# Kernel tuning notes

Hardware: AMD Instinct MI355X
Metric: run time of the kernel (lower is better)

The kernel has to match this reference:

```python
import jax, jax.numpy as jnp
import numpy as np

NLIG = 16384
NPROT = 131072
N = NLIG + NPROT
E = 2097152
B = 256
H = 64


def setup_inputs() -> dict:
    key = jax.random.key(0)
    ks = jax.random.split(key, 40)
    i = iter(range(40))

    def nrm(shape, scale=0.1):
        return (jax.random.normal(ks[next(i)], shape, jnp.float32) * scale)

    inp = {
        'lig_pos': nrm((NLIG, 3), 1.0),
        'lig_feat': nrm((NLIG, 15), 1.0),
        'prot_pos': nrm((NPROT, 3), 1.0),
        'prot_feat': nrm((NPROT, 8), 1.0),
        't': jax.random.uniform(ks[next(i)], (B,), jnp.float32) * 1000.0,
        'lig_batch': jnp.sort(jax.random.randint(ks[next(i)], (NLIG,), 0, B)),
        'prot_batch': jnp.sort(jax.random.randint(ks[next(i)], (NPROT,), 0, B)),
        'edge_index': jax.random.randint(ks[next(i)], (2, E), 0, N),
        'W_lig': nrm((15, H)), 'b_lig': nrm((H,)),
        'W_prot': nrm((8, H)), 'b_prot': nrm((H,)),
        'Wt1': nrm((H, H)), 'bt1': nrm((H,)),
        'Wt2': nrm((H, H)), 'bt2': nrm((H,)),
        'Wrel1': nrm((H, H)), 'brel1': nrm((H,)), 'Wroot1': nrm((H, H)),
        'Wrel2': nrm((H, H)), 'brel2': nrm((H,)), 'Wroot2': nrm((H, H)),
        'Wrel3': nrm((H, H)), 'brel3': nrm((H,)), 'Wroot3': nrm((H, H)),
        'Wro1': nrm((H, H)), 'bro1': nrm((H,)),
        'Wro2': nrm((H, 1)), 'bro2': nrm((1,)),
    }
    return inp


def _time_embedding(t, dim):
    half = dim // 2
    freqs = jnp.exp(jnp.arange(half, dtype=jnp.float32) * (-np.log(10000.0) / (half - 1)))
    e = t[:, None] * freqs[None, :]  # [B, half]
    return jnp.concatenate([jnp.sin(e), jnp.cos(e)], axis=-1)  # [B, dim]


def _silu(x):
    return x * jax.nn.sigmoid(x)


def _graph_conv(x, src, dst, Wrel, brel, Wroot):
    # PyG GraphConv (aggr='add'): lin_rel(sum_j x_j) + lin_root(x)
    agg = jax.ops.segment_sum(x[src], dst, num_segments=N)  # [N, H]
    return agg @ Wrel + brel + x @ Wroot


def reference(lig_pos, lig_feat, prot_pos, prot_feat, t, lig_batch, prot_batch,
              edge_index, W_lig, b_lig, W_prot, b_prot, Wt1, bt1, Wt2, bt2,
              Wrel1, brel1, Wroot1, Wrel2, brel2, Wroot2, Wrel3, brel3, Wroot3,
              Wro1, bro1, Wro2, bro2):
    t_emb = _time_embedding(t, H)                      # [B, H]
    t_emb = _silu(t_emb @ Wt1 + bt1) @ Wt2 + bt2       # time_mlp
    x_lig = lig_feat @ W_lig + b_lig + t_emb[lig_batch]
    x_prot = prot_feat @ W_prot + b_prot
    x = jnp.concatenate([x_lig, x_prot], axis=0)       # [N, H]

    src, dst = edge_index[0], edge_index[1]
    x = _graph_conv(x, src, dst, Wrel1, brel1, Wroot1)
    x = _graph_conv(x, src, dst, Wrel2, brel2, Wroot2)
    x = _graph_conv(x, src, dst, Wrel3, brel3, Wroot3)

    # global_mean_pool over ligand nodes
    lig_x = x[:NLIG]
    sums = jax.ops.segment_sum(lig_x, lig_batch, num_segments=B)  # [B, H]
    cnt = jax.ops.segment_sum(jnp.ones((NLIG,), jnp.float32), lig_batch, num_segments=B)
    pooled = sums / jnp.maximum(cnt, 1.0)[:, None]

    return _silu(pooled @ Wro1 + bro1) @ Wro2 + bro2   # [B, 1]
```

## Files before the change

kernel.cpp:

```cpp
#include <hip/hip_runtime.h>
#include <math.h>

#define NLIG 16384
#define NPROT 131072
#define NTOT (NLIG + NPROT)
#define NEDGE 2097152
#define NB 256
#define H 64
#define NBUCK 576
#define BSHIFT 8
#define BCAP 4608
#define NPW 24

typedef short v4s __attribute__((ext_vector_type(4)));
typedef float v4f __attribute__((ext_vector_type(4)));

__device__ __forceinline__ unsigned short f2bf(float f) {
    unsigned int u = __float_as_uint(f);
    u += 0x7fff + ((u >> 16) & 1);
    return (unsigned short)(u >> 16);
}
__device__ __forceinline__ float bf2f(unsigned short s) {
    return __uint_as_float(((unsigned int)s) << 16);
}
__device__ __forceinline__ float bflo(unsigned int u) {
    return __uint_as_float(u << 16);
}
__device__ __forceinline__ float bfhi(unsigned int u) {
    return __uint_as_float(u & 0xffff0000u);
}

__global__ __launch_bounds__(1024) void prep2_kernel(const float* __restrict__ t,
                                                     const float* __restrict__ Wt1, const float* __restrict__ bt1,
                                                     const float* __restrict__ Wt2, const float* __restrict__ bt2,
                                                     const float* __restrict__ W0, const float* __restrict__ W1,
                                                     const float* __restrict__ W2, const float* __restrict__ W3,
                                                     const float* __restrict__ W4, const float* __restrict__ W5,
                                                     unsigned short* __restrict__ wbuf,
                                                     float* __restrict__ t_emb,
                                                     unsigned int* __restrict__ zero_region) {
    int b = blockIdx.x, tid = threadIdx.x;
    if (b < 24) {
        const float* Ws[6] = {W0, W1, W2, W3, W4, W5};
        int tglob = b * 1024 + tid;
        int m = tglob >> 12, tt = tglob & 4095;
        int f = tt >> 8, l = (tt >> 2) & 63, i = tt & 3;
        int kt = f >> 2, ct = f & 3;
        int row = 16 * kt + 4 * (l >> 4) + i;
        int col = 16 * ct + (l & 15);
        wbuf[m * 4096 + tt] = f2bf(Ws[m][row * H + col]);
    } else if (b < 40) {
        __shared__ float emb_s[16][H];
        __shared__ float h1_s[16][H];
        int w = tid >> 6, h = tid & 63;
        int bb = (b - 24) * 16 + w;
        float tv = t[bb];
        int i = h & 31;
        float freq = expf((float)i * (-9.2103403719761836f / 31.0f));
        float e = tv * freq;
        emb_s[w][h] = (h < 32) ? sinf(e) : cosf(e);
        __syncthreads();
        float acc = bt1[h];
        #pragma unroll 8
        for (int k = 0; k < H; k++) acc += emb_s[w][k] * Wt1[k * H + h];
        float sig = 1.0f / (1.0f + expf(-acc));
        h1_s[w][h] = acc * sig;
        __syncthreads();
        float acc2 = bt2[h];
        #pragma unroll 8
        for (int k = 0; k < H; k++) acc2 += h1_s[w][k] * Wt2[k * H + h];
        t_emb[bb * H + h] = acc2;
    } else {
        for (int i = tid; i < 17216; i += 1024) zero_region[i] = 0;
    }
}

__global__ __launch_bounds__(1024) void fill_init_kernel(const int* __restrict__ edge_index,
                                                         unsigned int* __restrict__ bcursor,
                                                         unsigned int* __restrict__ bucketed,
                                                         const float* __restrict__ lig_feat,
                                                         const float* __restrict__ prot_feat,
                                                         const int* __restrict__ lig_batch,
                                                         const float* __restrict__ t_emb,
                                                         const float* __restrict__ W_lig,
                                                         const float* __restrict__ b_lig,
                                                         const float* __restrict__ W_prot,
                                                         const float* __restrict__ b_prot,
                                                         unsigned int* __restrict__ xb) {
    int b = blockIdx.x, tid = threadIdx.x;
    if (b < 256) {
        __shared__ unsigned int lh[NBUCK];
        __shared__ unsigned int lcur[NBUCK];
        __shared__ unsigned int gb[NBUCK];
        for (int i = tid; i < NBUCK; i += 1024) lh[i] = 0;
        __syncthreads();
        int e0 = b * 8192;
        int src[8], dst[8];
        #pragma unroll
        for (int k = 0; k < 8; k++) {
            src[k] = edge_index[e0 + k * 1024 + tid];
            dst[k] = edge_index[NEDGE + e0 + k * 1024 + tid];
            atomicAdd(&lh[dst[k] >> BSHIFT], 1);
        }
        __syncthreads();
        if (tid < NBUCK) {
            gb[tid] = atomicAdd(&bcursor[tid], lh[tid]);
            lcur[tid] = 0;
        }
        __syncthreads();
        #pragma unroll
        for (int k = 0; k < 8; k++) {
            int bb = dst[k] >> BSHIFT;
            unsigned int r = atomicAdd(&lcur[bb], 1);
            unsigned int slot = gb[bb] + r;
            if (slot < BCAP)
                bucketed[bb * BCAP + slot] =
                    (unsigned int)src[k] | ((unsigned int)(dst[k] & 255) << 18);
        }
    } else {
        int base = (b - 256) * 128;
        int h = tid & 63;
        #pragma unroll
        for (int it = 0; it < 8; it++) {
            int node = base + it * 16 + (tid >> 6);
            float acc;
            if (node < NLIG) {
                int bb = lig_batch[node];
                acc = b_lig[h] + t_emb[bb * H + h];
                #pragma unroll
                for (int k = 0; k < 15; k++)
                    acc += lig_feat[node * 15 + k] * W_lig[k * H + h];
            } else {
                int p = node - NLIG;
                acc = b_prot[h];
                #pragma unroll
                for (int k = 0; k < 8; k++)
                    acc += prot_feat[p * 8 + k] * W_prot[k * H + h];
            }
            float e0 = __shfl(acc, 2 * (h & 31));
            float e1 = __shfl(acc, 2 * (h & 31) + 1);
            if (h < 32)
                xb[node * 32 + h] = (unsigned int)f2bf(e0) | ((unsigned int)f2bf(e1) << 16);
        }
    }
}

__global__ __launch_bounds__(1024) void bucket_csr_kernel(const unsigned int* __restrict__ bucketed,
                                                          const unsigned int* __restrict__ bcursor,
                                                          int* __restrict__ off,
                                                          int* __restrict__ ends,
                                                          int* __restrict__ csr_src) {
    __shared__ unsigned int stage[BCAP];
    __shared__ unsigned int csr_l[BCAP];
    __shared__ unsigned int lh[256];
    __shared__ unsigned int sc[256];
    __shared__ unsigned int lcur[256];
    int b = blockIdx.x, tid = threadIdx.x;
    unsigned int base = (unsigned int)b * BCAP;
    int cnt = (int)bcursor[b];
    if (cnt > BCAP) cnt = BCAP;
    if (tid < 256) lh[tid] = 0;
    __syncthreads();
    for (int i = tid; i < cnt; i += 1024) {
        unsigned int v = bucketed[base + i];
        stage[i] = v;
        atomicAdd(&lh[v >> 18], 1);
    }
    __syncthreads();
    if (tid < 256) sc[tid] = lh[tid];
    __syncthreads();
    #pragma unroll
    for (int d = 1; d < 256; d <<= 1) {
        unsigned int v = (tid < 256 && tid >= (unsigned)d) ? sc[tid - d] : 0;
        __syncthreads();
        if (tid < 256) sc[tid] += v;
        __syncthreads();
    }
    if (tid < 256) {
        unsigned int excl = sc[tid] - lh[tid];
        lcur[tid] = excl;
        off[b * 256 + tid]  = (int)(base + excl);
        ends[b * 256 + tid] = (int)(base + excl + lh[tid]);
    }
    __syncthreads();
    for (int i = tid; i < cnt; i += 1024) {
        unsigned int v = stage[i];
        unsigned int p = atomicAdd(&lcur[v >> 18], 1);
        csr_l[p] = v & 0x3ffffu;
    }
    __syncthreads();
    for (int i = tid; i < cnt; i += 1024)
        csr_src[base + i] = (int)csr_l[i];
}

#define ACC8(u)                                   \
    do {                                          \
        a0 += bflo((u).x); a1 += bfhi((u).x);     \
        a2 += bflo((u).y); a3 += bfhi((u).y);     \
        a4 += bflo((u).z); a5 += bfhi((u).z);     \
        a6 += bflo((u).w); a7 += bfhi((u).w);     \
    } while (0)

#define DO_GROUP(BEG, DEG, IDFIRST, AGGROW)                                     \
    {                                                                           \
        int idcur = (IDFIRST);                                                  \
        float a0 = 0.f, a1 = 0.f, a2 = 0.f, a3 = 0.f;                           \
        float a4 = 0.f, a5 = 0.f, a6 = 0.f, a7 = 0.f;                           \
        for (int jb = 0; jb < (DEG); jb += 8) {                                 \
            int idnxt = (jb + 8 + q < (DEG)) ? csr[(BEG) + jb + 8 + q] : -1;    \
            int n0 = __shfl(idcur, s * 8 + 0);                                  \
            int n1 = __shfl(idcur, s * 8 + 1);                                  \
            int n2 = __shfl(idcur, s * 8 + 2);                                  \
            int n3 = __shfl(idcur, s * 8 + 3);                                  \
            int n4 = __shfl(idcur, s * 8 + 4);                                  \
            int n5 = __shfl(idcur, s * 8 + 5);                                  \
            int n6 = __shfl(idcur, s * 8 + 6);                                  \
            int n7 = __shfl(idcur, s * 8 + 7);                                  \
            int c1 = (n1 >= 0) ? n1 : n0;                                       \
            int c2 = (n2 >= 0) ? n2 : n0;                                       \
            int c3 = (n3 >= 0) ? n3 : n0;                                       \
            int c4 = (n4 >= 0) ? n4 : n0;                                       \
            int c5 = (n5 >= 0) ? n5 : n0;                                       \
            int c6 = (n6 >= 0) ? n6 : n0;                                       \
            int c7 = (n7 >= 0) ? n7 : n0;                                       \
            uint4 u0 = *(const uint4*)&xb[n0 * 32 + q * 4];                     \
            uint4 u1 = *(const uint4*)&xb[c1 * 32 + q * 4];                     \
            uint4 u2 = *(const uint4*)&xb[c2 * 32 + q * 4];                     \
            uint4 u3 = *(const uint4*)&xb[c3 * 32 + q * 4];                     \
            uint4 u4 = *(const uint4*)&xb[c4 * 32 + q * 4];                     \
            uint4 u5 = *(const uint4*)&xb[c5 * 32 + q * 4];                     \
            uint4 u6 = *(const uint4*)&xb[c6 * 32 + q * 4];                     \
            uint4 u7 = *(const uint4*)&xb[c7 * 32 + q * 4];                     \
            if (n1 < 0) { u1.x = u1.y = u1.z = u1.w = 0; }                      \
            if (n2 < 0) { u2.x = u2.y = u2.z = u2.w = 0; }                      \
            if (n3 < 0) { u3.x = u3.y = u3.z = u3.w = 0; }                      \
            if (n4 < 0) { u4.x = u4.y = u4.z = u4.w = 0; }                      \
            if (n5 < 0) { u5.x = u5.y = u5.z = u5.w = 0; }                      \
            if (n6 < 0) { u6.x = u6.y = u6.z = u6.w = 0; }                      \
            if (n7 < 0) { u7.x = u7.y = u7.z = u7.w = 0; }                      \
            ACC8(u0); ACC8(u1); ACC8(u2); ACC8(u3);                             \
            ACC8(u4); ACC8(u5); ACC8(u6); ACC8(u7);                             \
            idcur = idnxt;                                                      \
        }                                                                       \
        unsigned int p0 = (unsigned int)f2bf(a0) | ((unsigned int)f2bf(a1) << 16); \
        unsigned int p1 = (unsigned int)f2bf(a2) | ((unsigned int)f2bf(a3) << 16); \
        unsigned int p2 = (unsigned int)f2bf(a4) | ((unsigned int)f2bf(a5) << 16); \
        unsigned int p3 = (unsigned int)f2bf(a6) | ((unsigned int)f2bf(a7) << 16); \
        *(uint4*)&agg_s[(AGGROW) * 72 + q * 8] = make_uint4(p0, p1, p2, p3);    \
    }

__global__ __launch_bounds__(512, 6) void conv_kernel(const int* __restrict__ off,
                                                      const int* __restrict__ ends,
                                                      const int* __restrict__ csr,
                                                      const unsigned int* __restrict__ xb,
                                                      const unsigned short* __restrict__ wbuf,
                                                      const float* __restrict__ brel,
                                                      unsigned int* __restrict__ xob) {
    __shared__ unsigned int wlds[4096];
    __shared__ unsigned short agg_s[8 * NPW * 72];
    const int tid = threadIdx.x;
    const int w = tid >> 6, l = tid & 63;
    const unsigned int* wsrc = (const unsigned int*)wbuf;
    #pragma unroll
    for (int i = 0; i < 8; i++) wlds[i * 512 + tid] = wsrc[i * 512 + tid];

    const int s = l >> 3, q = l & 7;
    const int lrow = l & 15, g16 = l >> 4, g4 = 4 * (l >> 4);
    const int gwid = blockIdx.x * 8 + w;
    const int node0w = gwid * NPW;

    int bvv = (l < NPW) ? off[node0w + l] : 0;
    int evv = (l < NPW) ? ends[node0w + l] : 0;

    int b0 = __shfl(bvv, s),      d0 = __shfl(evv, s) - b0;
    int b1 = __shfl(bvv, 8 + s),  d1 = __shfl(evv, 8 + s) - b1;
    int b2 = __shfl(bvv, 16 + s), d2 = __shfl(evv, 16 + s) - b2;
    int id0 = (q < d0) ? csr[b0 + q] : -1;
    int id1 = (q < d1) ? csr[b1 + q] : -1;
    int id2 = (q < d2) ? csr[b2 + q] : -1;

    __syncthreads();

    float bv[4];
    #pragma unroll
    for (int ct = 0; ct < 4; ct++) bv[ct] = brel[ct * 16 + lrow];

    DO_GROUP(b0, d0, id0, w * NPW + s)
    DO_GROUP(b1, d1, id1, w * NPW + 8 + s)
    DO_GROUP(b2, d2, id2, w * NPW + 16 + s)

    __builtin_amdgcn_wave_barrier();

    v4s ax[4];
    #pragma unroll
    for (int kt = 0; kt < 4; kt++)
        ax[kt] = *(const v4s*)&xb[(node0w + lrow) * 32 + kt * 8 + g16 * 2];
    v4f acc[4];
    #pragma unroll
    for (int ct = 0; ct < 4; ct++) acc[ct] = (v4f){0.f, 0.f, 0.f, 0.f};
    #pragma unroll
    for (int kt = 0; kt < 4; kt++) {
        v4s a_agg = *(const v4s*)&agg_s[(w * NPW + lrow) * 72 + kt * 16 + g4];
        #pragma unroll
        for (int ct = 0; ct < 4; ct++) {
            int f = kt * 4 + ct;
            v4s wr = *(const v4s*)&wlds[f * 128 + l * 2];
            v4s wo = *(const v4s*)&wlds[2048 + f * 128 + l * 2];
            acc[ct] = __builtin_amdgcn_mfma_f32_16x16x16bf16_1k(a_agg, wr, acc[ct], 0, 0, 0);
            acc[ct] = __builtin_amdgcn_mfma_f32_16x16x16bf16_1k(ax[kt], wo, acc[ct], 0, 0, 0);
        }
    }
    const int r2row = 16 + (l & 7);
    v4s ax2[4];
    #pragma unroll
    for (int kt = 0; kt < 4; kt++)
        ax2[kt] = *(const v4s*)&xb[(node0w + r2row) * 32 + kt * 8 + g16 * 2];
    v4f acc2[4];
    #pragma unroll
    for (int ct = 0; ct < 4; ct++) acc2[ct] = (v4f){0.f, 0.f, 0.f, 0.f};
    #pragma unroll
    for (int kt = 0; kt < 4; kt++) {
        v4s a_agg2 = *(const v4s*)&agg_s[(w * NPW + r2row) * 72 + kt * 16 + g4];
        #pragma unroll
        for (int ct = 0; ct < 4; ct++) {
            int f = kt * 4 + ct;
            v4s wr = *(const v4s*)&wlds[f * 128 + l * 2];
            v4s wo = *(const v4s*)&wlds[2048 + f * 128 + l * 2];
            acc2[ct] = __builtin_amdgcn_mfma_f32_16x16x16bf16_1k(a_agg2, wr, acc2[ct], 0, 0, 0);
            acc2[ct] = __builtin_amdgcn_mfma_f32_16x16x16bf16_1k(ax2[kt], wo, acc2[ct], 0, 0, 0);
        }
    }
    __builtin_amdgcn_wave_barrier();

    #pragma unroll
    for (int ct = 0; ct < 4; ct++) {
        #pragma unroll
        for (int r = 0; r < 4; r++)
            agg_s[(w * NPW + g4 + r) * 72 + ct * 16 + lrow] = f2bf(acc[ct][r] + bv[ct]);
    }
    if (g16 < 2) {
        #pragma unroll
        for (int ct = 0; ct < 4; ct++) {
            #pragma unroll
            for (int r = 0; r < 4; r++)
                agg_s[(w * NPW + 16 + g4 + r) * 72 + ct * 16 + lrow] =
                    f2bf(acc2[ct][r] + bv[ct]);
        }
    }
    __builtin_amdgcn_wave_barrier();

    {
        int row = l >> 2, qq = l & 3;
        const unsigned int* srcp = (const unsigned int*)&agg_s[(w * NPW + row) * 72 + qq * 16];
        uint4 v0 = *(const uint4*)(srcp);
        uint4 v1 = *(const uint4*)(srcp + 4);
        *(uint4*)&xob[(node0w + row) * 32 + qq * 8] = v0;
        *(uint4*)&xob[(node0w + row) * 32 + qq * 8 + 4] = v1;
    }
    {
        int row = 16 + (l >> 3), qq = l & 7;
        *(uint4*)&xob[(node0w + row) * 32 + qq * 4] =
            *(const uint4*)&agg_s[(w * NPW + row) * 72 + qq * 8];
    }
}

__global__ __launch_bounds__(512, 6) void conv_lig_kernel(const int* __restrict__ off,
                                                          const int* __restrict__ ends,
                                                          const int* __restrict__ csr,
                                                          const unsigned int* __restrict__ xb,
                                                          const unsigned short* __restrict__ wbuf,
                                                          const float* __restrict__ brel,
                                                          const int* __restrict__ lig_batch,
                                                          float* __restrict__ pooled,
                                                          float* __restrict__ cnt) {
    __shared__ unsigned int wlds[4096];
    __shared__ unsigned short agg_s[8 * 8 * 72];
    const int tid = threadIdx.x;
    const int w = tid >> 6, l = tid & 63;
    const unsigned int* wsrc = (const unsigned int*)wbuf;
    #pragma unroll
    for (int i = 0; i < 8; i++) wlds[i * 512 + tid] = wsrc[i * 512 + tid];

    const int s = l >> 3, q = l & 7;
    const int lrow = l & 15, g16 = l >> 4, g4 = 4 * (l >> 4);
    const int gwid = blockIdx.x * 8 + w;
    const int node0w = gwid * 8;

    int bvv = (l < 8) ? off[node0w + l] : 0;
    int evv = (l < 8) ? ends[node0w + l] : 0;
    int b0 = __shfl(bvv, s), d0 = __shfl(evv, s) - b0;
    int id0 = (q < d0) ? csr[b0 + q] : -1;

    __syncthreads();

    float bv[4];
    #pragma unroll
    for (int ct = 0; ct < 4; ct++) bv[ct] = brel[ct * 16 + lrow];

    DO_GROUP(b0, d0, id0, w * 8 + s)

    __builtin_amdgcn_wave_barrier();

    const int arow = lrow & 7;
    v4s ax[4];
    #pragma unroll
    for (int kt = 0; kt < 4; kt++)
        ax[kt] = *(const v4s*)&xb[(node0w + arow) * 32 + kt * 8 + g16 * 2];
    v4f acc[4];
    #pragma unroll
    for (int ct = 0; ct < 4; ct++) acc[ct] = (v4f){0.f, 0.f, 0.f, 0.f};
    #pragma unroll
    for (int kt = 0; kt < 4; kt++) {
        v4s a_agg = *(const v4s*)&agg_s[(w * 8 + arow) * 72 + kt * 16 + g4];
        #pragma unroll
        for (int ct = 0; ct < 4; ct++) {
            int f = kt * 4 + ct;
            v4s wr = *(const v4s*)&wlds[f * 128 + l * 2];
            v4s wo = *(const v4s*)&wlds[2048 + f * 128 + l * 2];
            acc[ct] = __builtin_amdgcn_mfma_f32_16x16x16bf16_1k(a_agg, wr, acc[ct], 0, 0, 0);
            acc[ct] = __builtin_amdgcn_mfma_f32_16x16x16bf16_1k(ax[kt], wo, acc[ct], 0, 0, 0);
        }
    }

    if (g16 < 2) {
        #pragma unroll
        for (int r = 0; r < 4; r++) {
            int node = node0w + g4 + r;
            int bb = lig_batch[node];
            #pragma unroll
            for (int ct = 0; ct < 4; ct++)
                unsafeAtomicAdd(&pooled[bb * H + ct * 16 + lrow], acc[ct][r] + bv[ct]);
            if (lrow == 0) unsafeAtomicAdd(&cnt[bb], 1.0f);
        }
    }
}

__global__ void readout_kernel(const float* __restrict__ pooled, const float* __restrict__ cnt,
                               const float* __restrict__ Wro1, const float* __restrict__ bro1,
                               const float* __restrict__ Wro2, const float* __restrict__ bro2,
                               float* __restrict__ out) {
    __shared__ float pm[4][H];
    int w = threadIdx.x >> 6;
    int h = threadIdx.x & 63;
    int b = blockIdx.x * 4 + w;
    float c = fmaxf(cnt[b], 1.0f);
    pm[w][h] = pooled[b * H + h] / c;
    __syncthreads();
    float acc = bro1[h];
    #pragma unroll 8
    for (int k = 0; k < H; k++) acc += pm[w][k] * Wro1[k * H + h];
    float sig = 1.0f / (1.0f + expf(-acc));
    float s = acc * sig;
    float r = s * Wro2[h];
    #pragma unroll
    for (int off = 32; off; off >>= 1) r += __shfl_down(r, off);
    if (h == 0) out[b] = r + bro2[0];
}

extern "C" void kernel_launch(void* const* d_in, const int* in_sizes, int n_in,
                              void* d_out, int out_size, void* d_ws, size_t ws_size,
                              hipStream_t stream) {
    const float* lig_feat  = (const float*)d_in[1];
    const float* prot_feat = (const float*)d_in[3];
    const float* t         = (const float*)d_in[4];
    const int*   lig_batch = (const int*)d_in[5];
    const int*   edge_index= (const int*)d_in[7];
    const float* W_lig  = (const float*)d_in[8];
    const float* b_lig  = (const float*)d_in[9];
    const float* W_prot = (const float*)d_in[10];
    const float* b_prot = (const float*)d_in[11];
    const float* Wt1 = (const float*)d_in[12];
    const float* bt1 = (const float*)d_in[13];
    const float* Wt2 = (const float*)d_in[14];
    const float* bt2 = (const float*)d_in[15];
    const float* Wrel[3]  = {(const float*)d_in[16], (const float*)d_in[19], (const float*)d_in[22]};
    const float* brel[3]  = {(const float*)d_in[17], (const float*)d_in[20], (const float*)d_in[23]};
    const float* Wroot[3] = {(const float*)d_in[18], (const float*)d_in[21], (const float*)d_in[24]};
    const float* Wro1 = (const float*)d_in[25];
    const float* bro1 = (const float*)d_in[26];
    const float* Wro2 = (const float*)d_in[27];
    const float* bro2 = (const float*)d_in[28];
    float* out = (float*)d_out;

    char* ws = (char*)d_ws;
    int*            off_a   = (int*)(ws);
    int*            ends_a  = (int*)(ws + 655360);
    unsigned int*   bcursor = (unsigned int*)(ws + 1310720);
    float*          pooled  = (float*)(ws + 1313024);
    float*          cnt     = (float*)(ws + 1378560);
    float*          t_emb   = (float*)(ws + 1380352);
    unsigned short* wbuf    = (unsigned short*)(ws + 1572864);
    int*            csr_src = (int*)(ws + 2097152);
    unsigned int*   bucketed= (unsigned int*)(ws + 14680064);
    unsigned int*   xb0     = (unsigned int*)(ws + 27262976);
    unsigned int*   xb1     = (unsigned int*)(ws + 46137344);

    prep2_kernel<<<41, 1024, 0, stream>>>(t, Wt1, bt1, Wt2, bt2,
                                          Wrel[0], Wroot[0], Wrel[1], Wroot[1], Wrel[2], Wroot[2],
                                          wbuf, t_emb, bcursor);

    fill_init_kernel<<<256 + NTOT / 128, 1024, 0, stream>>>(edge_index, bcursor, bucketed,
                                                            lig_feat, prot_feat, lig_batch, t_emb,
                                                            W_lig, b_lig, W_prot, b_prot, xb0);

    bucket_csr_kernel<<<NBUCK, 1024, 0, stream>>>(bucketed, bcursor, off_a, ends_a, csr_src);

    conv_kernel<<<768, 512, 0, stream>>>(off_a, ends_a, csr_src, xb0,
                                         wbuf, brel[0], xb1);
    conv_kernel<<<768, 512, 0, stream>>>(off_a, ends_a, csr_src, xb1,
                                         wbuf + 8192, brel[1], xb0);
    conv_lig_kernel<<<NLIG / 64, 512, 0, stream>>>(off_a, ends_a, csr_src, xb0,
                                                   wbuf + 16384, brel[2], lig_batch,
                                                   pooled, cnt);

    readout_kernel<<<NB / 4, 256, 0, stream>>>(pooled, cnt, Wro1, bro1, Wro2, bro2, out);
}
```

Baseline: 210.4 us.

## Use per-wavefront LDS histograms and interleave bucket and init blocks

```diff
diff --git a/kernel.cpp b/kernel.cpp
--- a/kernel.cpp
+++ b/kernel.cpp
@@ -88,37 +88,46 @@
                                                          const float* __restrict__ b_prot,
                                                          unsigned int* __restrict__ xb) {
     int b = blockIdx.x, tid = threadIdx.x;
-    if (b < 256) {
-        __shared__ unsigned int lh[NBUCK];
-        __shared__ unsigned int lcur[NBUCK];
+    int grp = b / 11, pos = b - grp * 11;
+    if (pos < 2) {
+        __shared__ unsigned int seg[16 * NBUCK];
         __shared__ unsigned int gb[NBUCK];
-        for (int i = tid; i < NBUCK; i += 1024) lh[i] = 0;
-        __syncthreads();
-        int e0 = b * 8192;
+        int fid = grp * 2 + pos;
+        int w = tid >> 6;
+        for (int i = tid; i < 16 * NBUCK; i += 1024) seg[i] = 0;
+        __syncthreads();
+        int e0 = fid * 8192;
         int src[8], dst[8];
         #pragma unroll
         for (int k = 0; k < 8; k++) {
             src[k] = edge_index[e0 + k * 1024 + tid];
             dst[k] = edge_index[NEDGE + e0 + k * 1024 + tid];
-            atomicAdd(&lh[dst[k] >> BSHIFT], 1);
+            atomicAdd(&seg[w * NBUCK + (dst[k] >> BSHIFT)], 1);
         }
         __syncthreads();
         if (tid < NBUCK) {
-            gb[tid] = atomicAdd(&bcursor[tid], lh[tid]);
-            lcur[tid] = 0;
+            unsigned int tot = 0;
+            #pragma unroll
+            for (int ww = 0; ww < 16; ww++) {
+                unsigned int c = seg[ww * NBUCK + tid];
+                seg[ww * NBUCK + tid] = tot;
+                tot += c;
+            }
+            gb[tid] = atomicAdd(&bcursor[tid], tot);
         }
         __syncthreads();
         #pragma unroll
         for (int k = 0; k < 8; k++) {
             int bb = dst[k] >> BSHIFT;
-            unsigned int r = atomicAdd(&lcur[bb], 1);
+            unsigned int r = atomicAdd(&seg[w * NBUCK + bb], 1);
             unsigned int slot = gb[bb] + r;
             if (slot < BCAP)
                 bucketed[bb * BCAP + slot] =
                     (unsigned int)src[k] | ((unsigned int)(dst[k] & 255) << 18);
         }
     } else {
-        int base = (b - 256) * 128;
+        int ib = grp * 9 + (pos - 2);
+        int base = ib * 128;
         int h = tid & 63;
         #pragma unroll
         for (int it = 0; it < 8; it++) {
@@ -152,22 +161,31 @@
                                                           int* __restrict__ csr_src) {
     __shared__ unsigned int stage[BCAP];
     __shared__ unsigned int csr_l[BCAP];
-    __shared__ unsigned int lh[256];
+    __shared__ unsigned int seg[16 * 256];
     __shared__ unsigned int sc[256];
-    __shared__ unsigned int lcur[256];
     int b = blockIdx.x, tid = threadIdx.x;
+    int w = tid >> 6;
     unsigned int base = (unsigned int)b * BCAP;
     int cnt = (int)bcursor[b];
     if (cnt > BCAP) cnt = BCAP;
-    if (tid < 256) lh[tid] = 0;
+    for (int i = tid; i < 16 * 256; i += 1024) seg[i] = 0;
     __syncthreads();
     for (int i = tid; i < cnt; i += 1024) {
         unsigned int v = bucketed[base + i];
         stage[i] = v;
-        atomicAdd(&lh[v >> 18], 1);
-    }
-    __syncthreads();
-    if (tid < 256) sc[tid] = lh[tid];
+        atomicAdd(&seg[w * 256 + (v >> 18)], 1);
+    }
+    __syncthreads();
+    unsigned int tot = 0;
+    if (tid < 256) {
+        #pragma unroll
+        for (int ww = 0; ww < 16; ww++) {
+            unsigned int c = seg[ww * 256 + tid];
+            seg[ww * 256 + tid] = tot;
+            tot += c;
+        }
+        sc[tid] = tot;
+    }
     __syncthreads();
     #pragma unroll
     for (int d = 1; d < 256; d <<= 1) {
@@ -177,15 +195,16 @@
         __syncthreads();
     }
     if (tid < 256) {
-        unsigned int excl = sc[tid] - lh[tid];
-        lcur[tid] = excl;
+        unsigned int excl = sc[tid] - tot;
         off[b * 256 + tid]  = (int)(base + excl);
-        ends[b * 256 + tid] = (int)(base + excl + lh[tid]);
+        ends[b * 256 + tid] = (int)(base + excl + tot);
+        #pragma unroll
+        for (int ww = 0; ww < 16; ww++) seg[ww * 256 + tid] += excl;
     }
     __syncthreads();
     for (int i = tid; i < cnt; i += 1024) {
         unsigned int v = stage[i];
-        unsigned int p = atomicAdd(&lcur[v >> 18], 1);
+        unsigned int p = atomicAdd(&seg[w * 256 + (v >> 18)], 1);
         csr_l[p] = v & 0x3ffffu;
     }
     __syncthreads();
@@ -499,9 +518,9 @@
                                           Wrel[0], Wroot[0], Wrel[1], Wroot[1], Wrel[2], Wroot[2],
                                           wbuf, t_emb, bcursor);
 
-    fill_init_kernel<<<256 + NTOT / 128, 1024, 0, stream>>>(edge_index, bcursor, bucketed,
-                                                            lig_feat, prot_feat, lig_batch, t_emb,
-                                                            W_lig, b_lig, W_prot, b_prot, xb0);
+    fill_init_kernel<<<1408, 1024, 0, stream>>>(edge_index, bcursor, bucketed,
+                                                lig_feat, prot_feat, lig_batch, t_emb,
+                                                W_lig, b_lig, W_prot, b_prot, xb0);
 
     bucket_csr_kernel<<<NBUCK, 1024, 0, stream>>>(bucketed, bcursor, off_a, ends_a, csr_src);
 
```

New measurement: 205.5 us. -2.3%, faster.
